# Performance work log

Measured on AMD Instinct MI355X. Metric: run time of the kernel, lower is better.

Reference implementation:

```python
import jax, jax.numpy as jnp
import numpy as np


def _degree(idx, n):
    # number of edges touching each node, clamped to >=1 (DGL GraphConv behavior)
    d = jax.ops.segment_sum(jnp.ones(idx.shape[0], jnp.float32), idx, num_segments=n)
    return jnp.maximum(d, 1.0)


def _graph_conv(x, src, dst, W, b):
    # DGL GraphConv, norm='both':  out = D_in^{-1/2} A (D_out^{-1/2} x) W + b
    n = x.shape[0]
    cj = jax.lax.rsqrt(_degree(src, n))[:, None]  # source (out-degree) norm
    ci = jax.lax.rsqrt(_degree(dst, n))[:, None]  # dest (in-degree) norm
    h = (x * cj) @ W                              # mult W first (order-invariant math)
    agg = jax.ops.segment_sum(h[src], dst, num_segments=n)  # SpMM: gather + scatter-add
    return agg * ci + b


def setup_inputs() -> dict:
    key = jax.random.key(0)
    ks = jax.random.split(key, 8)
    N, E, G = 50000, 800000, 64
    de, u, da, L = 128, 256, 256, 50
    x = jax.random.normal(ks[0], (N, de), jnp.float32)
    src = jax.random.randint(ks[1], (E,), 0, N, jnp.int32)
    dst = jax.random.randint(ks[2], (E,), 0, N, jnp.int32)
    graph_ids = jnp.sort(jax.random.randint(ks[3], (N,), 0, G, jnp.int32))
    W1 = jax.random.normal(ks[4], (de, u), jnp.float32) / np.sqrt(de)
    b1 = jnp.zeros((u,), jnp.float32)
    W2 = jax.random.normal(ks[5], (u, da), jnp.float32) / np.sqrt(u)
    b2 = jnp.zeros((da,), jnp.float32)
    Wl = jax.random.normal(ks[6], (da, L), jnp.float32) / np.sqrt(da)
    bl = jnp.zeros((L,), jnp.float32)
    return {"x": x, "src": src, "dst": dst, "graph_ids": graph_ids,
            "num_graphs": G, "W1": W1, "b1": b1, "W2": W2, "b2": b2,
            "Wl": Wl, "bl": bl}


def reference(x, src, dst, graph_ids, num_graphs, W1, b1, W2, b2, Wl, bl):
    h = _graph_conv(x, src, dst, W1, b1)
    h = jax.nn.relu(h)                      # dropout is identity in eval mode
    h = _graph_conv(h, src, dst, W2, b2)
    # dgl.mean_nodes: ragged segment-mean readout over batched graphs
    sums = jax.ops.segment_sum(h, graph_ids, num_segments=num_graphs)
    cnts = jax.ops.segment_sum(jnp.ones(h.shape[0], jnp.float32), graph_ids,
                               num_segments=num_graphs)
    hg = sums / jnp.maximum(cnts, 1.0)[:, None]  # [G, da]
    return hg @ Wl + bl                          # [G, L] label logits
```

## Files before the change

kernel.cpp:

```cpp
#include <hip/hip_runtime.h>
#include <cstdint>


typedef __attribute__((ext_vector_type(8))) short short8v;
typedef __attribute__((ext_vector_type(4))) float f32x4;

constexpr int RSPLIT = 4;
constexpr int BSLICE = 64;
constexpr int LDSN = 12544;

static __device__ __forceinline__ unsigned f2bf(float f) {
  unsigned u = __float_as_uint(f);
  u += 0x7FFFu + ((u >> 16) & 1u);
  return u >> 16;
}
static __device__ __forceinline__ float bf2f(unsigned h) {
  return __uint_as_float(h << 16);
}

__global__ __launch_bounds__(256)
void k_setup(const int* __restrict__ src, const int* __restrict__ dst,
             const float* __restrict__ W1, const float* __restrict__ W2,
             const float* __restrict__ Wl, const float* __restrict__ b2,
             const float* __restrict__ bl,
             unsigned short* __restrict__ outpart, unsigned short* __restrict__ inpart,
             unsigned short* __restrict__ BT1, float* __restrict__ Wc,
             float* __restrict__ cb, int* __restrict__ counter,
             int E, int N, int L) {
  __shared__ int cnt_s[LDSN];
  __shared__ float w2row[256];
  const int blk = blockIdx.x;
  const int tid = threadIdx.x;
  if (blk == 0 && tid == 0) *counter = 0;

  if (blk < 2 * RSPLIT * BSLICE) {
    const int h = blk >> 8;
    const int sub = blk & 255;
    const int b = sub >> 2, r = sub & 3;
    const int* idx = h ? dst : src;
    unsigned short* part = h ? inpart : outpart;
    const int RN = (N + RSPLIT - 1) / RSPLIT;
    const int r0 = r * RN;
    int rlen = N - r0; if (rlen > RN) rlen = RN; if (rlen < 0) rlen = 0;
    for (int i = tid; i < rlen; i += 256) cnt_s[i] = 0;
    __syncthreads();
    const int e0 = (int)((long long)E * b / BSLICE);
    const int e1 = (int)((long long)E * (b + 1) / BSLICE);
    for (int e = e0 + tid; e < e1; e += 256) {
      int v = idx[e] - r0;
      if (v >= 0 && v < rlen) atomicAdd(&cnt_s[v], 1);
    }
    __syncthreads();
    unsigned short* dp = part + (size_t)b * N + r0;
    for (int i = tid; i < rlen; i += 256) dp[i] = (unsigned short)cnt_s[i];
  } else if (blk < 2 * RSPLIT * BSLICE + 128) {
    int i = (blk - 512) * 256 + tid;
    int k = i >> 8, nn = i & 255;
    BT1[(size_t)nn * 128 + k] = (unsigned short)f2bf(W1[i]);
  } else {
    int c = blk - (2 * RSPLIT * BSLICE + 128);
    if (c < 256) {
      w2row[tid] = W2[(size_t)c * 256 + tid];
      __syncthreads();
      int l = tid;
      if (l < L) {
        float a = 0.f;
#pragma unroll 8
        for (int m = 0; m < 256; ++m) a += w2row[m] * Wl[(size_t)m * L + l];
        Wc[(size_t)c * L + l] = a;
      }
    } else {
      int l = tid;
      if (l < L) {
        float a = bl[l];
#pragma unroll 8
        for (int m = 0; m < 256; ++m) a += b2[m] * Wl[(size_t)m * L + l];
        cb[l] = a;
      }
    }
  }
}

__global__ void k_norms(const unsigned short* __restrict__ outpart,
                        const unsigned short* __restrict__ inpart,
                        float* __restrict__ cj, float* __restrict__ ci,
                        int* __restrict__ indeg_tot, int* __restrict__ row_start,
                        int* __restrict__ cursor_base, int* __restrict__ counter, int N) {
  int i = blockIdx.x * blockDim.x + threadIdx.x;
  int din = 0, dout = 0;
  if (i < N) {
    for (int b = 0; b < BSLICE; ++b) {
      din += inpart[(size_t)b * N + i];
      dout += outpart[(size_t)b * N + i];
    }
    cj[i] = rsqrtf((float)(dout > 1 ? dout : 1));
    ci[i] = rsqrtf((float)(din  > 1 ? din  : 1));
    indeg_tot[i] = din;
  }
  int lane = threadIdx.x & 63;
  int inc = din;
#pragma unroll
  for (int off = 1; off < 64; off <<= 1) {
    int o = __shfl_up(inc, off);
    if (lane >= off) inc += o;
  }
  int excl = inc - din;
  int wsum = __shfl(inc, 63);
  int base = 0;
  if (lane == 0) base = atomicAdd(counter, wsum);
  base = __shfl(base, 0);
  if (i < N) {
    int rs = base + excl;
    row_start[i] = rs;
    for (int b = 0; b < BSLICE; ++b) {
      cursor_base[(size_t)b * N + i] = rs;
      rs += inpart[(size_t)b * N + i];
    }
  }
}

__global__ __launch_bounds__(256)
void k_fillcast(const int* __restrict__ src, const int* __restrict__ dst,
                const int* __restrict__ cursor_base, int* __restrict__ csr_src,
                const float4* __restrict__ x, const float* __restrict__ cj,
                unsigned short* __restrict__ xb, int E, int N) {
  __shared__ int cur_s[LDSN];
  const int blk = blockIdx.x;
  if (blk < RSPLIT * BSLICE) {
    const int b = blk >> 2, r = blk & 3;
    const int RN = (N + RSPLIT - 1) / RSPLIT;
    const int r0 = r * RN;
    int rlen = N - r0; if (rlen > RN) rlen = RN; if (rlen < 0) rlen = 0;
    const int* cb_ = cursor_base + (size_t)b * N + r0;
    for (int i = threadIdx.x; i < rlen; i += 256) cur_s[i] = cb_[i];
    __syncthreads();
    const int e0 = (int)((long long)E * b / BSLICE);
    const int e1 = (int)((long long)E * (b + 1) / BSLICE);
    for (int e = e0 + (int)threadIdx.x; e < e1; e += 256) {
      int d = dst[e] - r0;
      if (d >= 0 && d < rlen) {
        int pos = atomicAdd(&cur_s[d], 1);
        csr_src[pos] = src[e];
      }
    }
  } else {
    int i = (blk - RSPLIT * BSLICE) * 256 + (int)threadIdx.x;
    if (i < N * 32) {
      float c = cj[i >> 5];
      float4 v = x[i];
      uint2 r;
      r.x = f2bf(c * v.x) | (f2bf(c * v.y) << 16);
      r.y = f2bf(c * v.z) | (f2bf(c * v.w) << 16);
      *(uint2*)(xb + (size_t)i * 4) = r;
    }
  }
}

__global__ __launch_bounds__(256)
void k_spmm(const unsigned* __restrict__ feat,
            const int* __restrict__ row_start, const int* __restrict__ cnts,
            const int* __restrict__ csr_src, unsigned* __restrict__ out, int N) {
  const int n = blockIdx.x * 4 + (threadIdx.x >> 6);
  if (n >= N) return;
  const int t = threadIdx.x & 63;
  const int beg = __builtin_amdgcn_readfirstlane(row_start[n]);
  const int cnt = __builtin_amdgcn_readfirstlane(cnts[n]);
  float acc0 = 0.f, acc1 = 0.f;

  for (int k = 0; k < cnt; k += 8) {
    int s[8];
#pragma unroll
    for (int u = 0; u < 8; ++u) {
      int kk = k + u;
      s[u] = csr_src[beg + (kk < cnt ? kk : cnt - 1)];
    }
    unsigned w[8];
#pragma unroll
    for (int u = 0; u < 8; ++u) w[u] = feat[(size_t)s[u] * 64 + t];
#pragma unroll
    for (int u = 0; u < 8; ++u) {
      if (k + u >= cnt) w[u] = 0;
      acc0 += bf2f(w[u] & 0xFFFF);
      acc1 += bf2f(w[u] >> 16);
    }
  }
  out[(size_t)n * 64 + t] = f2bf(acc0) | (f2bf(acc1) << 16);
}

__global__ __launch_bounds__(256, 2)
void k_gemm_mfma(const unsigned short* __restrict__ A, const unsigned short* __restrict__ BT,
                 const float* __restrict__ ci, const float* __restrict__ bias,
                 const float* __restrict__ cjv, unsigned short* __restrict__ out, int M) {
  constexpr int K = 128;
  __shared__ unsigned short Bs[64 * 64 * 8];
  const int tid = threadIdx.x;
  const int lane = tid & 63;
  const int wave = tid >> 6;
  const int l15 = lane & 15;
  const int kA = (lane >> 4) * 8;

#pragma unroll
  for (int it = 0; it < 16; ++it) {
    int c = it * 256 + tid;
    int f = c >> 6, l = c & 63;
    int ct = f & 15, kb = f >> 4;
    int col = ct * 16 + (l & 15);
    int ko = kb * 32 + (l >> 4) * 8;
    *(uint4*)&Bs[(size_t)c * 8] = *(const uint4*)(BT + (size_t)col * K + ko);
  }
  __syncthreads();

  const int rowW = blockIdx.x * 128 + wave * 32;
  const unsigned short* aP0 = A + (size_t)(rowW + l15) * K + kA;
  const unsigned short* aP1 = aP0 + (size_t)16 * K;

  short8v a0[4], a1[4];
#pragma unroll
  for (int kb = 0; kb < 4; ++kb) {
    a0[kb] = *(const short8v*)(aP0 + kb * 32);
    a1[kb] = *(const short8v*)(aP1 + kb * 32);
  }

  f32x4 acc0[16], acc1[16];
#pragma unroll
  for (int i = 0; i < 16; ++i) {
    acc0[i] = (f32x4){0.f, 0.f, 0.f, 0.f};
    acc1[i] = (f32x4){0.f, 0.f, 0.f, 0.f};
  }

  const unsigned short* bL = Bs + lane * 8;
#pragma unroll
  for (int kb = 0; kb < 4; ++kb) {
#pragma unroll
    for (int ct = 0; ct < 16; ++ct) {
      short8v bv = *(const short8v*)(bL + (size_t)(kb * 16 + ct) * 512);
      acc0[ct] = __builtin_amdgcn_mfma_f32_16x16x32_bf16(a0[kb], bv, acc0[ct], 0, 0, 0);
      acc1[ct] = __builtin_amdgcn_mfma_f32_16x16x32_bf16(a1[kb], bv, acc1[ct], 0, 0, 0);
    }
  }

#pragma unroll
  for (int half = 0; half < 2; ++half) {
    const f32x4* acc = half ? acc1 : acc0;
    const int row0 = rowW + (lane >> 4) * 4 + half * 16;
    float cir[4], cjr[4];
#pragma unroll
    for (int r = 0; r < 4; ++r) {
      int rI = row0 + r; if (rI > M - 1) rI = M - 1;
      cir[r] = ci[rI];
      cjr[r] = cjv[rI];
    }
    unsigned short* ob = out + (size_t)(row0 >> 3) * 2048 + (row0 & 7);
#pragma unroll
    for (int ct = 0; ct < 16; ++ct) {
      int col = ct * 16 + l15;
      float bb = bias[col];
      unsigned h0 = f2bf(fmaxf(acc[ct][0] * cir[0] + bb, 0.f) * cjr[0]);
      unsigned h1 = f2bf(fmaxf(acc[ct][1] * cir[1] + bb, 0.f) * cjr[1]);
      unsigned h2 = f2bf(fmaxf(acc[ct][2] * cir[2] + bb, 0.f) * cjr[2]);
      unsigned h3 = f2bf(fmaxf(acc[ct][3] * cir[3] + bb, 0.f) * cjr[3]);
      uint2 pk;
      pk.x = h0 | (h1 << 16);
      pk.y = h2 | (h3 << 16);
      *(uint2*)(ob + (size_t)col * 8) = pk;
    }
  }
}

__global__ __launch_bounds__(256)
void k_wgn(const int* __restrict__ gids, const float* __restrict__ ci,
           const int* __restrict__ row_start, const int* __restrict__ cnts,
           const int* __restrict__ csr_src, float* __restrict__ Wg,
           int N, int Npad, int G) {
  __shared__ float row_s[LDSN];
  const int g = blockIdx.x % G;
  const int r = blockIdx.x / G;
  const int RNW = (Npad + RSPLIT - 1) / RSPLIT;
  const int r0 = r * RNW;
  int rlen = Npad - r0; if (rlen > RNW) rlen = RNW; if (rlen < 0) rlen = 0;
  for (int i = threadIdx.x; i < rlen; i += 256) row_s[i] = 0.f;
  __syncthreads();
  int lo = 0, hi = N;
  while (lo < hi) { int m = (lo + hi) >> 1; if (gids[m] < g) lo = m + 1; else hi = m; }
  int lo2 = lo, hi2 = N;
  while (lo2 < hi2) { int m = (lo2 + hi2) >> 1; if (gids[m] < g + 1) lo2 = m + 1; else hi2 = m; }
  for (int n = lo + (int)threadIdx.x; n < lo2; n += 256) {
    float cin = ci[n];
    int beg = row_start[n];
    int cnt = cnts[n];
    for (int k = 0; k < cnt; ++k) {
      int s = csr_src[beg + k] - r0;
      if (s >= 0 && s < rlen) atomicAdd(&row_s[s], cin);
    }
  }
  __syncthreads();
  float* wr = Wg + (size_t)g * Npad + r0;
  for (int i = threadIdx.x; i < rlen; i += 256) wr[i] = row_s[i];
}

__global__ __launch_bounds__(256)
void k_tgemm(const float* __restrict__ Wg, const unsigned short* __restrict__ h1t8,
             float* __restrict__ tpart, int Npad) {
  __shared__ unsigned short As[64][136];
  const int tid = threadIdx.x;
  const int lane = tid & 63;
  const int wv = tid >> 6;
  const int l15 = lane & 15;
  const int kA = (lane >> 4) * 8;

  f32x4 acc[16];
#pragma unroll
  for (int i = 0; i < 16; ++i) acc[i] = (f32x4){0.f, 0.f, 0.f, 0.f};

  const int kbeg = blockIdx.x * 256;
#pragma unroll
  for (int step = 0; step < 2; ++step) {
    int k0 = kbeg + step * 128;
    if (k0 >= Npad) break;
#pragma unroll
    for (int it = 0; it < 8; ++it) {
      int idx = it * 256 + tid;
      int r = idx >> 5, q = idx & 31;
      float4 v = *(const float4*)(Wg + (size_t)r * Npad + k0 + q * 4);
      uint2 pk;
      pk.x = f2bf(v.x) | (f2bf(v.y) << 16);
      pk.y = f2bf(v.z) | (f2bf(v.w) << 16);
      *(uint2*)&As[r][q * 4] = pk;
    }
    __syncthreads();
#pragma unroll
    for (int sub = 0; sub < 4; ++sub) {
      short8v a[4];
#pragma unroll
      for (int m = 0; m < 4; ++m)
        a[m] = *(const short8v*)&As[m * 16 + l15][sub * 32 + kA];
      int kk = k0 + sub * 32 + kA;
      const unsigned short* bp = h1t8 + (size_t)(kk >> 3) * 2048;
#pragma unroll
      for (int n = 0; n < 4; ++n) {
        int col = wv * 64 + n * 16 + l15;
        short8v bv = *(const short8v*)(bp + (size_t)col * 8);
#pragma unroll
        for (int m = 0; m < 4; ++m)
          acc[m * 4 + n] = __builtin_amdgcn_mfma_f32_16x16x32_bf16(a[m], bv, acc[m * 4 + n], 0, 0, 0);
      }
    }
    __syncthreads();
  }

  float* tp = tpart + (size_t)blockIdx.x * 16384;
  const int grp = lane >> 4;
#pragma unroll
  for (int m = 0; m < 4; ++m)
#pragma unroll
    for (int n = 0; n < 4; ++n) {
      int col = wv * 64 + n * 16 + l15;
      f32x4 v = acc[m * 4 + n];
#pragma unroll
      for (int r = 0; r < 4; ++r)
        tp[(size_t)(m * 16 + grp * 4 + r) * 256 + col] = v[r];
    }
}

__global__ __launch_bounds__(256)
void k_tred(const float* __restrict__ tpart, float* __restrict__ t2, int NB, int NCH) {
  int g = blockIdx.x & 63;
  int chunk = blockIdx.x >> 6;
  int c = threadIdx.x;
  float s = 0.f;
  for (int b = chunk; b < NB; b += NCH)
    s += tpart[(size_t)b * 16384 + g * 256 + c];
  t2[((size_t)chunk * 64 + g) * 256 + c] = s;
}

__global__ __launch_bounds__(256)
void k_final2(const float* __restrict__ t2, const int* __restrict__ gids,
              const float* __restrict__ Wc, const float* __restrict__ cb,
              const float* __restrict__ bl, float* __restrict__ out,
              int N, int L, int NCH) {
  int g = blockIdx.x;
  __shared__ float ts[256];
  int c = threadIdx.x;
  float s = 0.f;
  for (int ch = 0; ch < NCH; ++ch) s += t2[((size_t)ch * 64 + g) * 256 + c];
  ts[c] = s;
  int lo = 0, hi = N;
  while (lo < hi) { int m = (lo + hi) >> 1; if (gids[m] < g) lo = m + 1; else hi = m; }
  int lo2 = lo, hi2 = N;
  while (lo2 < hi2) { int m = (lo2 + hi2) >> 1; if (gids[m] < g + 1) lo2 = m + 1; else hi2 = m; }
  int cnt = lo2 - lo;
  float inv = 1.0f / (float)(cnt > 1 ? cnt : 1);
  __syncthreads();
  if (c < L) {
    float a = 0.f;
    for (int k = 0; k < 256; ++k) a += ts[k] * Wc[(size_t)k * L + c];
    out[(size_t)g * L + c] = a * inv + (cnt > 0 ? cb[c] : bl[c]);
  }
}

static inline size_t alignup(size_t v) { return (v + 255) & ~(size_t)255; }

extern "C" void kernel_launch(void* const* d_in, const int* in_sizes, int n_in,
                              void* d_out, int out_size, void* d_ws, size_t ws_size,
                              hipStream_t stream) {
  const float* x   = (const float*)d_in[0];
  const int*   src = (const int*)d_in[1];
  const int*   dst = (const int*)d_in[2];
  const int*   gid = (const int*)d_in[3];
  const float* W1  = (const float*)d_in[5];
  const float* b1  = (const float*)d_in[6];
  const float* W2  = (const float*)d_in[7];
  const float* b2  = (const float*)d_in[8];
  const float* Wl  = (const float*)d_in[9];
  const float* bl  = (const float*)d_in[10];
  float* out = (float*)d_out;

  const int N  = in_sizes[3];
  const int E  = in_sizes[1];
  const int L  = in_sizes[10];
  const int G  = out_size / L;
  const int RB = (N + 127) / 128;
  const int Npad = RB * 128;
  const int NB = (Npad + 255) / 256;
  const int NCH = 16;

  char* p = (char*)d_ws;
  int*   counter    = (int*)p;   p += 256;
  unsigned short* outpart = (unsigned short*)p; p += alignup((size_t)BSLICE * N * 2);
  unsigned short* inpart  = (unsigned short*)p; p += alignup((size_t)BSLICE * N * 2);
  int*   cursor_base= (int*)p;   p += alignup((size_t)BSLICE * N * 4);
  int*   indeg_tot  = (int*)p;   p += alignup((size_t)N * 4);
  float* cj         = (float*)p; p += alignup((size_t)N * 4);
  float* ci         = (float*)p; p += alignup((size_t)N * 4);
  int*   row_start  = (int*)p;   p += alignup((size_t)N * 4);
  int*   csr_src    = (int*)p;   p += alignup((size_t)E * 4);
  unsigned short* xb = (unsigned short*)p; p += alignup((size_t)Npad * 128 * 2);
  unsigned short* a1 = (unsigned short*)p; p += alignup((size_t)Npad * 128 * 2);
  unsigned short* h1t8 = (unsigned short*)p; p += alignup((size_t)Npad * 256 * 2);
  unsigned short* BT1  = (unsigned short*)p; p += alignup((size_t)256 * 128 * 2);
  float* Wg         = (float*)p; p += alignup((size_t)G * Npad * 4);
  float* tpart      = (float*)p; p += alignup((size_t)NB * 64 * 256 * 4);
  float* t2         = (float*)p; p += alignup((size_t)NCH * 64 * 256 * 4);
  float* Wc         = (float*)p; p += alignup((size_t)256 * L * 4);
  float* cb         = (float*)p; p += alignup((size_t)L * 4);
  (void)ws_size; (void)n_in;

  const int SETUP_BLOCKS = 2 * RSPLIT * BSLICE + 128 + 257;
  k_setup<<<SETUP_BLOCKS, 256, 0, stream>>>(src, dst, W1, W2, Wl, b2, bl,
                                            outpart, inpart, BT1, Wc, cb,
                                            counter, E, N, L);

  k_norms<<<(N + 255) / 256, 256, 0, stream>>>(outpart, inpart, cj, ci, indeg_tot,
                                               row_start, cursor_base, counter, N);

  const int FC_BLOCKS = RSPLIT * BSLICE + (N * 32 + 255) / 256;
  k_fillcast<<<FC_BLOCKS, 256, 0, stream>>>(src, dst, cursor_base, csr_src,
                                            (const float4*)x, cj, xb, E, N);

  k_spmm<<<(N + 3) / 4, 256, 0, stream>>>((const unsigned*)xb, row_start, indeg_tot,
                                          csr_src, (unsigned*)a1, N);

  k_gemm_mfma<<<RB, 256, 0, stream>>>(a1, BT1, ci, b1, cj, h1t8, N);

  k_wgn<<<RSPLIT * G, 256, 0, stream>>>(gid, ci, row_start, indeg_tot, csr_src,
                                        Wg, N, Npad, G);

  k_tgemm<<<NB, 256, 0, stream>>>(Wg, h1t8, tpart, Npad);

  k_tred<<<NCH * 64, 256, 0, stream>>>(tpart, t2, NB, NCH);

  k_final2<<<G, 256, 0, stream>>>(t2, gid, Wc, cb, bl, out, N, L, NCH);
}
```

Before: 199.4 us.

## Merge layer-1 GEMM and per-graph weight kernel; pack degree histogram counters

The layer-1 MFMA GEMM and the per-graph aggregation-weight kernel become one launch, with block index choosing the role, so the two independent jobs run side by side and one launch is saved. The degree histogram now packs two 16-bit counters per LDS word, so each block covers half the node range and the histogram needs half as many blocks, each rescanning its edge slice fewer times. Packed 16-bit counters could overflow on very high-degree nodes within one slice. The merged kernel uses launch_bounds(256,2), which may limit occupancy for the weight-scatter blocks.

```diff
diff --git a/kernel.cpp b/kernel.cpp
--- a/kernel.cpp
+++ b/kernel.cpp
@@ -6,8 +6,10 @@
 typedef __attribute__((ext_vector_type(4))) float f32x4;
 
 constexpr int RSPLIT = 4;
+constexpr int HSPLIT = 2;
 constexpr int BSLICE = 64;
 constexpr int LDSN = 12544;
+constexpr int LDSH = 12544;
 
 static __device__ __forceinline__ unsigned f2bf(float f) {
   unsigned u = __float_as_uint(f);
@@ -27,38 +29,41 @@
              unsigned short* __restrict__ BT1, float* __restrict__ Wc,
              float* __restrict__ cb, int* __restrict__ counter,
              int E, int N, int L) {
-  __shared__ int cnt_s[LDSN];
+  __shared__ unsigned cnt_s[LDSH];
   __shared__ float w2row[256];
   const int blk = blockIdx.x;
   const int tid = threadIdx.x;
   if (blk == 0 && tid == 0) *counter = 0;
 
-  if (blk < 2 * RSPLIT * BSLICE) {
-    const int h = blk >> 8;
-    const int sub = blk & 255;
-    const int b = sub >> 2, r = sub & 3;
+  const int NHIST = 2 * BSLICE * HSPLIT;
+  if (blk < NHIST) {
+    const int h = blk >> 7;
+    const int sub = blk & 127;
+    const int b = sub >> 1, r = sub & 1;
     const int* idx = h ? dst : src;
     unsigned short* part = h ? inpart : outpart;
-    const int RN = (N + RSPLIT - 1) / RSPLIT;
+    const int RN = (N + HSPLIT - 1) / HSPLIT;
     const int r0 = r * RN;
     int rlen = N - r0; if (rlen > RN) rlen = RN; if (rlen < 0) rlen = 0;
-    for (int i = tid; i < rlen; i += 256) cnt_s[i] = 0;
+    const int words = (rlen + 1) >> 1;
+    for (int i = tid; i < words; i += 256) cnt_s[i] = 0;
     __syncthreads();
     const int e0 = (int)((long long)E * b / BSLICE);
     const int e1 = (int)((long long)E * (b + 1) / BSLICE);
     for (int e = e0 + tid; e < e1; e += 256) {
       int v = idx[e] - r0;
-      if (v >= 0 && v < rlen) atomicAdd(&cnt_s[v], 1);
-    }
-    __syncthreads();
-    unsigned short* dp = part + (size_t)b * N + r0;
-    for (int i = tid; i < rlen; i += 256) dp[i] = (unsigned short)cnt_s[i];
-  } else if (blk < 2 * RSPLIT * BSLICE + 128) {
-    int i = (blk - 512) * 256 + tid;
+      if (v >= 0 && v < rlen)
+        atomicAdd(&cnt_s[v >> 1], 1u << ((v & 1) * 16));
+    }
+    __syncthreads();
+    unsigned* dp = (unsigned*)(part + (size_t)b * N + r0);
+    for (int i = tid; i < words; i += 256) dp[i] = cnt_s[i];
+  } else if (blk < NHIST + 128) {
+    int i = (blk - NHIST) * 256 + tid;
     int k = i >> 8, nn = i & 255;
     BT1[(size_t)nn * 128 + k] = (unsigned short)f2bf(W1[i]);
   } else {
-    int c = blk - (2 * RSPLIT * BSLICE + 128);
+    int c = blk - (NHIST + 128);
     if (c < 256) {
       w2row[tid] = W2[(size_t)c * 256 + tid];
       __syncthreads();
@@ -188,114 +193,116 @@
 }
 
 __global__ __launch_bounds__(256, 2)
-void k_gemm_mfma(const unsigned short* __restrict__ A, const unsigned short* __restrict__ BT,
-                 const float* __restrict__ ci, const float* __restrict__ bias,
-                 const float* __restrict__ cjv, unsigned short* __restrict__ out, int M) {
-  constexpr int K = 128;
+void k_gw(const unsigned short* __restrict__ A, const unsigned short* __restrict__ BT,
+          const float* __restrict__ ci, const float* __restrict__ bias,
+          const float* __restrict__ cjv, unsigned short* __restrict__ out, int M,
+          const int* __restrict__ gids, const int* __restrict__ row_start,
+          const int* __restrict__ cnts, const int* __restrict__ csr_src,
+          float* __restrict__ Wg, int Npad, int G, int RB) {
   __shared__ unsigned short Bs[64 * 64 * 8];
   const int tid = threadIdx.x;
-  const int lane = tid & 63;
-  const int wave = tid >> 6;
-  const int l15 = lane & 15;
-  const int kA = (lane >> 4) * 8;
-
-#pragma unroll
-  for (int it = 0; it < 16; ++it) {
-    int c = it * 256 + tid;
-    int f = c >> 6, l = c & 63;
-    int ct = f & 15, kb = f >> 4;
-    int col = ct * 16 + (l & 15);
-    int ko = kb * 32 + (l >> 4) * 8;
-    *(uint4*)&Bs[(size_t)c * 8] = *(const uint4*)(BT + (size_t)col * K + ko);
-  }
-  __syncthreads();
-
-  const int rowW = blockIdx.x * 128 + wave * 32;
-  const unsigned short* aP0 = A + (size_t)(rowW + l15) * K + kA;
-  const unsigned short* aP1 = aP0 + (size_t)16 * K;
-
-  short8v a0[4], a1[4];
-#pragma unroll
-  for (int kb = 0; kb < 4; ++kb) {
-    a0[kb] = *(const short8v*)(aP0 + kb * 32);
-    a1[kb] = *(const short8v*)(aP1 + kb * 32);
-  }
-
-  f32x4 acc0[16], acc1[16];
-#pragma unroll
-  for (int i = 0; i < 16; ++i) {
-    acc0[i] = (f32x4){0.f, 0.f, 0.f, 0.f};
-    acc1[i] = (f32x4){0.f, 0.f, 0.f, 0.f};
-  }
-
-  const unsigned short* bL = Bs + lane * 8;
-#pragma unroll
-  for (int kb = 0; kb < 4; ++kb) {
-#pragma unroll
-    for (int ct = 0; ct < 16; ++ct) {
-      short8v bv = *(const short8v*)(bL + (size_t)(kb * 16 + ct) * 512);
-      acc0[ct] = __builtin_amdgcn_mfma_f32_16x16x32_bf16(a0[kb], bv, acc0[ct], 0, 0, 0);
-      acc1[ct] = __builtin_amdgcn_mfma_f32_16x16x32_bf16(a1[kb], bv, acc1[ct], 0, 0, 0);
-    }
-  }
-
-#pragma unroll
-  for (int half = 0; half < 2; ++half) {
-    const f32x4* acc = half ? acc1 : acc0;
-    const int row0 = rowW + (lane >> 4) * 4 + half * 16;
-    float cir[4], cjr[4];
-#pragma unroll
-    for (int r = 0; r < 4; ++r) {
-      int rI = row0 + r; if (rI > M - 1) rI = M - 1;
-      cir[r] = ci[rI];
-      cjr[r] = cjv[rI];
-    }
-    unsigned short* ob = out + (size_t)(row0 >> 3) * 2048 + (row0 & 7);
-#pragma unroll
-    for (int ct = 0; ct < 16; ++ct) {
-      int col = ct * 16 + l15;
-      float bb = bias[col];
-      unsigned h0 = f2bf(fmaxf(acc[ct][0] * cir[0] + bb, 0.f) * cjr[0]);
-      unsigned h1 = f2bf(fmaxf(acc[ct][1] * cir[1] + bb, 0.f) * cjr[1]);
-      unsigned h2 = f2bf(fmaxf(acc[ct][2] * cir[2] + bb, 0.f) * cjr[2]);
-      unsigned h3 = f2bf(fmaxf(acc[ct][3] * cir[3] + bb, 0.f) * cjr[3]);
-      uint2 pk;
-      pk.x = h0 | (h1 << 16);
-      pk.y = h2 | (h3 << 16);
-      *(uint2*)(ob + (size_t)col * 8) = pk;
-    }
-  }
-}
-
-__global__ __launch_bounds__(256)
-void k_wgn(const int* __restrict__ gids, const float* __restrict__ ci,
-           const int* __restrict__ row_start, const int* __restrict__ cnts,
-           const int* __restrict__ csr_src, float* __restrict__ Wg,
-           int N, int Npad, int G) {
-  __shared__ float row_s[LDSN];
-  const int g = blockIdx.x % G;
-  const int r = blockIdx.x / G;
-  const int RNW = (Npad + RSPLIT - 1) / RSPLIT;
-  const int r0 = r * RNW;
-  int rlen = Npad - r0; if (rlen > RNW) rlen = RNW; if (rlen < 0) rlen = 0;
-  for (int i = threadIdx.x; i < rlen; i += 256) row_s[i] = 0.f;
-  __syncthreads();
-  int lo = 0, hi = N;
-  while (lo < hi) { int m = (lo + hi) >> 1; if (gids[m] < g) lo = m + 1; else hi = m; }
-  int lo2 = lo, hi2 = N;
-  while (lo2 < hi2) { int m = (lo2 + hi2) >> 1; if (gids[m] < g + 1) lo2 = m + 1; else hi2 = m; }
-  for (int n = lo + (int)threadIdx.x; n < lo2; n += 256) {
-    float cin = ci[n];
-    int beg = row_start[n];
-    int cnt = cnts[n];
-    for (int k = 0; k < cnt; ++k) {
-      int s = csr_src[beg + k] - r0;
-      if (s >= 0 && s < rlen) atomicAdd(&row_s[s], cin);
-    }
-  }
-  __syncthreads();
-  float* wr = Wg + (size_t)g * Npad + r0;
-  for (int i = threadIdx.x; i < rlen; i += 256) wr[i] = row_s[i];
+
+  if ((int)blockIdx.x < RB) {
+    constexpr int K = 128;
+    const int lane = tid & 63;
+    const int wave = tid >> 6;
+    const int l15 = lane & 15;
+    const int kA = (lane >> 4) * 8;
+
+#pragma unroll
+    for (int it = 0; it < 16; ++it) {
+      int c = it * 256 + tid;
+      int f = c >> 6, l = c & 63;
+      int ct = f & 15, kb = f >> 4;
+      int col = ct * 16 + (l & 15);
+      int ko = kb * 32 + (l >> 4) * 8;
+      *(uint4*)&Bs[(size_t)c * 8] = *(const uint4*)(BT + (size_t)col * K + ko);
+    }
+    __syncthreads();
+
+    const int rowW = blockIdx.x * 128 + wave * 32;
+    const unsigned short* aP0 = A + (size_t)(rowW + l15) * K + kA;
+    const unsigned short* aP1 = aP0 + (size_t)16 * K;
+
+    short8v a0[4], a1v[4];
+#pragma unroll
+    for (int kb = 0; kb < 4; ++kb) {
+      a0[kb] = *(const short8v*)(aP0 + kb * 32);
+      a1v[kb] = *(const short8v*)(aP1 + kb * 32);
+    }
+
+    f32x4 acc0[16], acc1[16];
+#pragma unroll
+    for (int i = 0; i < 16; ++i) {
+      acc0[i] = (f32x4){0.f, 0.f, 0.f, 0.f};
+      acc1[i] = (f32x4){0.f, 0.f, 0.f, 0.f};
+    }
+
+    const unsigned short* bL = Bs + lane * 8;
+#pragma unroll
+    for (int kb = 0; kb < 4; ++kb) {
+#pragma unroll
+      for (int ct = 0; ct < 16; ++ct) {
+        short8v bv = *(const short8v*)(bL + (size_t)(kb * 16 + ct) * 512);
+        acc0[ct] = __builtin_amdgcn_mfma_f32_16x16x32_bf16(a0[kb], bv, acc0[ct], 0, 0, 0);
+        acc1[ct] = __builtin_amdgcn_mfma_f32_16x16x32_bf16(a1v[kb], bv, acc1[ct], 0, 0, 0);
+      }
+    }
+
+#pragma unroll
+    for (int half = 0; half < 2; ++half) {
+      const f32x4* acc = half ? acc1 : acc0;
+      const int row0 = rowW + (lane >> 4) * 4 + half * 16;
+      float cir[4], cjr[4];
+#pragma unroll
+      for (int r = 0; r < 4; ++r) {
+        int rI = row0 + r; if (rI > M - 1) rI = M - 1;
+        cir[r] = ci[rI];
+        cjr[r] = cjv[rI];
+      }
+      unsigned short* ob = out + (size_t)(row0 >> 3) * 2048 + (row0 & 7);
+#pragma unroll
+      for (int ct = 0; ct < 16; ++ct) {
+        int col = ct * 16 + l15;
+        float bb = bias[col];
+        unsigned h0 = f2bf(fmaxf(acc[ct][0] * cir[0] + bb, 0.f) * cjr[0]);
+        unsigned h1 = f2bf(fmaxf(acc[ct][1] * cir[1] + bb, 0.f) * cjr[1]);
+        unsigned h2 = f2bf(fmaxf(acc[ct][2] * cir[2] + bb, 0.f) * cjr[2]);
+        unsigned h3 = f2bf(fmaxf(acc[ct][3] * cir[3] + bb, 0.f) * cjr[3]);
+        uint2 pk;
+        pk.x = h0 | (h1 << 16);
+        pk.y = h2 | (h3 << 16);
+        *(uint2*)(ob + (size_t)col * 8) = pk;
+      }
+    }
+  } else {
+    float* row_s = (float*)Bs;
+    const int bid = (int)blockIdx.x - RB;
+    const int g = bid % G;
+    const int r = bid / G;
+    const int RNW = (Npad + RSPLIT - 1) / RSPLIT;
+    const int r0 = r * RNW;
+    int rlen = Npad - r0; if (rlen > RNW) rlen = RNW; if (rlen < 0) rlen = 0;
+    for (int i = tid; i < rlen; i += 256) row_s[i] = 0.f;
+    __syncthreads();
+    int N_ = M;
+    int lo = 0, hi = N_;
+    while (lo < hi) { int m = (lo + hi) >> 1; if (gids[m] < g) lo = m + 1; else hi = m; }
+    int lo2 = lo, hi2 = N_;
+    while (lo2 < hi2) { int m = (lo2 + hi2) >> 1; if (gids[m] < g + 1) lo2 = m + 1; else hi2 = m; }
+    for (int n = lo + tid; n < lo2; n += 256) {
+      float cin = ci[n];
+      int beg = row_start[n];
+      int cnt = cnts[n];
+      for (int k = 0; k < cnt; ++k) {
+        int s = csr_src[beg + k] - r0;
+        if (s >= 0 && s < rlen) atomicAdd(&row_s[s], cin);
+      }
+    }
+    __syncthreads();
+    float* wr = Wg + (size_t)g * Npad + r0;
+    for (int i = tid; i < rlen; i += 256) wr[i] = row_s[i];
+  }
 }
 
 __global__ __launch_bounds__(256)
@@ -445,7 +452,7 @@
   float* cb         = (float*)p; p += alignup((size_t)L * 4);
   (void)ws_size; (void)n_in;
 
-  const int SETUP_BLOCKS = 2 * RSPLIT * BSLICE + 128 + 257;
+  const int SETUP_BLOCKS = 2 * BSLICE * HSPLIT + 128 + 257;
   k_setup<<<SETUP_BLOCKS, 256, 0, stream>>>(src, dst, W1, W2, Wl, b2, bl,
                                             outpart, inpart, BT1, Wc, cb,
                                             counter, E, N, L);
@@ -460,10 +467,9 @@
   k_spmm<<<(N + 3) / 4, 256, 0, stream>>>((const unsigned*)xb, row_start, indeg_tot,
                                           csr_src, (unsigned*)a1, N);
 
-  k_gemm_mfma<<<RB, 256, 0, stream>>>(a1, BT1, ci, b1, cj, h1t8, N);
-
-  k_wgn<<<RSPLIT * G, 256, 0, stream>>>(gid, ci, row_start, indeg_tot, csr_src,
-                                        Wg, N, Npad, G);
+  k_gw<<<RB + RSPLIT * G, 256, 0, stream>>>(a1, BT1, ci, b1, cj, h1t8, N,
+                                            gid, row_start, indeg_tot, csr_src,
+                                            Wg, Npad, G, RB);
 
   k_tgemm<<<NB, 256, 0, stream>>>(Wg, h1t8, tpart, Npad);
 
```

Result: faster. 192.1 us, median of 2 (-3.7%).
